# Kernel tuning notes

Hardware: AMD Instinct MI355X
Metric: run time of the kernel (lower is better)

## Reference

```python
import jax, jax.numpy as jnp
import numpy as np

DEPTH = 4
HEADS = 8
DIM = 512
DIM_HEAD = 64
INNER = HEADS * DIM_HEAD  # 512
MLP = 2048
NPK = 32
NEG = -1e9
EPS = 1e-5


def setup_inputs() -> dict:
    key = jax.random.key(0)
    ks = jax.random.split(key, 12)
    b, n, k = 2, 4096, 144
    x = jax.random.normal(ks[0], (b, n, DIM), jnp.float32)
    kx = jax.random.normal(ks[1], (b, k, DIM), jnp.float32)
    rd = jax.random.uniform(ks[2], (b, k, n), jnp.float32)
    clst = jax.random.normal(ks[3], (b, 1, DIM), jnp.float32)
    mask = jax.random.uniform(ks[4], (b, n, 1), jnp.float32)
    kmask = jax.random.uniform(ks[5], (b, k, 1), jnp.float32)

    def init(kk, shape, fan):
        return jax.random.normal(kk, shape, jnp.float32) / np.float32(np.sqrt(fan))

    return {
        "x": x, "kx": kx, "rd": rd, "clst": clst, "mask": mask, "kmask": kmask,
        "ln1_g": jnp.ones((DEPTH, DIM), jnp.float32),
        "ln1_b": jnp.zeros((DEPTH, DIM), jnp.float32),
        "w_qkv": init(ks[6], (DEPTH, DIM, 3 * INNER), DIM),
        "w_out": init(ks[7], (DEPTH, INNER, DIM), INNER),
        "b_out": jnp.zeros((DEPTH, DIM), jnp.float32),
        "ln2_g": jnp.ones((DEPTH, DIM), jnp.float32),
        "ln2_b": jnp.zeros((DEPTH, DIM), jnp.float32),
        "w1": init(ks[8], (DEPTH, DIM, MLP), DIM),
        "b1": jnp.zeros((DEPTH, MLP), jnp.float32),
        "w2": init(ks[9], (DEPTH, MLP, DIM), MLP),
        "b2": jnp.zeros((DEPTH, DIM), jnp.float32),
    }


def _ln(t, g, b):
    m = jnp.mean(t, axis=-1, keepdims=True)
    v = jnp.mean(jnp.square(t - m), axis=-1, keepdims=True)
    return (t - m) / jnp.sqrt(v + EPS) * g + b


def _split_heads(t):
    b, n, _ = t.shape
    return t.reshape(b, n, HEADS, DIM_HEAD).transpose(0, 2, 1, 3)  # b h n d


def _merge_heads(t):
    b, h, n, d = t.shape
    return t.transpose(0, 2, 1, 3).reshape(b, n, h * d)


def reference(x, kx, rd, clst, mask, kmask,
              ln1_g, ln1_b, w_qkv, w_out, b_out,
              ln2_g, ln2_b, w1, b1, w2, b2):
    scale = DIM_HEAD ** -0.5
    kernel_mask = kmask < 0.5                                   # [b,k,1] -> broadcast over dim
    att_mask = (jnp.einsum('bid,bjd->bij', mask, kmask) < 0.5)[:, None]  # [b,1,n,k]
    rd2 = (rd * rd)[:, None]                                    # [b,1,k,n]

    k_reps = []
    for l in range(DEPTH):
        x = _ln(x, ln1_g[l], ln1_b[l])
        kx = _ln(kx, ln1_g[l], ln1_b[l])
        clst = _ln(clst, ln1_g[l], ln1_b[l])
        krd = jnp.exp(-rd2 / (2 * NPK * (2 ** l)))              # [b,1,k,n]

        def qkv(t):
            p = t @ w_qkv[l]
            q, kk, v = jnp.split(p, 3, axis=-1)
            return _split_heads(q), _split_heads(kk), _split_heads(v)

        t_q, t_k, t_v = qkv(x)
        k_q, k_k, k_v = qkv(kx)
        c_q, _, _ = qkv(clst)

        def to_out(t):
            return _merge_heads(t) @ w_out[l] + b_out[l]

        # patch -> kernel cross-attention with post-softmax decay
        dots = jnp.einsum('bhid,bhjd->bhij', t_q, k_k) * scale   # [b,h,n,k]
        dots = jnp.where(att_mask, NEG, dots)
        attn = jax.nn.softmax(dots, axis=-1) * jnp.swapaxes(krd, -1, -2)
        x_ = to_out(jnp.einsum('bhij,bhjd->bhid', attn, k_v))

        # kernel -> patch cross-attention with decay
        k_dots = jnp.einsum('bhid,bhjd->bhij', k_q, t_k) * scale  # [b,h,k,n]
        k_dots = jnp.where(jnp.swapaxes(att_mask, -1, -2), NEG, k_dots)
        k_attn = jax.nn.softmax(k_dots, axis=-1) * krd
        kx_ = to_out(jnp.einsum('bhij,bhjd->bhid', k_attn, t_v))

        # class token -> kernel attention (no decay)
        c_dots = jnp.einsum('bhid,bhjd->bhij', c_q, k_k) * scale  # [b,h,1,k]
        c_dots = jnp.where(att_mask[:, :, :1], NEG, c_dots)
        c_attn = jax.nn.softmax(c_dots, axis=-1)
        clst_ = to_out(jnp.einsum('bhij,bhjd->bhid', c_attn, k_v))

        x = x + x_
        clst = clst + clst_
        kx = kx + kx_

        def ff(t):
            h = _ln(t, ln2_g[l], ln2_b[l])
            h = jax.nn.gelu(h @ w1[l] + b1[l], approximate=False)
            return h @ w2[l] + b2[l]

        x = ff(x) + x
        clst = ff(clst) + clst
        kx = ff(kx) + kx
        k_reps.append(jnp.where(kernel_mask, 0.0, kx))

    return jnp.stack(k_reps), clst
```

## Files before the change

### kernel.cpp

```cpp
#include <hip/hip_runtime.h>
#include <hip/hip_bf16.h>
#include <math.h>

#define NPAT 4096
#define NKER 144
#define DIMC 512
#define QKV_N 1536
#define MLP_N 2048
#define R_TOT 8482
#define R_PAD 8576
#define ROW_KX 8192
#define ROW_C 8480

typedef __hip_bfloat16 bf16;
using f32x4 = __attribute__((ext_vector_type(4))) float;
using s16x8 = __attribute__((ext_vector_type(8))) short;

template<typename T> __device__ __forceinline__ float tof(T v);
template<> __device__ __forceinline__ float tof<float>(float v) { return v; }
template<> __device__ __forceinline__ float tof<bf16>(bf16 v) { return __bfloat162float(v); }
template<typename T> __device__ __forceinline__ T fromf(float v);
template<> __device__ __forceinline__ float fromf<float>(float v) { return v; }
template<> __device__ __forceinline__ bf16 fromf<bf16>(float v) { return __float2bfloat16(v); }

__device__ __forceinline__ void gload_lds16(const bf16* g, bf16* l) {
  __builtin_amdgcn_global_load_lds((const __attribute__((address_space(1))) void*)g,
                                   (__attribute__((address_space(3))) void*)l, 16, 0, 0);
}

__device__ __forceinline__ float gelu_f(float x) {
  float u = 0.7978845608028654f * (x + 0.044715f * x * x * x);
  float t = 2.f / (1.f + __expf(-2.f * u)) - 1.f;
  return 0.5f * x * (1.f + t);
}

__device__ __forceinline__ unsigned fenc(float f) {
  unsigned u = __float_as_uint(f);
  return (u & 0x80000000u) ? ~u : (u | 0x80000000u);
}
__device__ __forceinline__ float fdec(unsigned u) {
  return (u & 0x80000000u) ? __uint_as_float(u & 0x7FFFFFFFu) : __uint_as_float(~u);
}

__device__ __forceinline__ float dot64q(const float* __restrict__ q, const bf16* __restrict__ k) {
  float acc = 0.f;
  const uint4* k4 = (const uint4*)k;
  #pragma unroll
  for (int t = 0; t < 8; ++t) {
    union { uint4 u; bf16 h[8]; } w; w.u = k4[t];
    #pragma unroll
    for (int e = 0; e < 8; ++e) acc += q[t * 8 + e] * tof(w.h[e]);
  }
  return acc;
}

template<typename TD>
__global__ void cvt_in(const float* __restrict__ s, TD* __restrict__ d, int n) {
  int i = blockIdx.x * 256 + threadIdx.x;
  if (i < n) d[i] = fromf<TD>(s[i]);
}

__global__ __launch_bounds__(256) void transpose_cvt(const float* __restrict__ src,
    bf16* __restrict__ dst, int K, int N) {
  __shared__ float tile[32][33];
  int kb = blockIdx.y * 32, nb = blockIdx.x * 32;
  int tx = threadIdx.x & 31, ty = threadIdx.x >> 5;
  #pragma unroll
  for (int r = ty; r < 32; r += 8) tile[r][tx] = src[(size_t)(kb + r) * N + nb + tx];
  __syncthreads();
  #pragma unroll
  for (int r = ty; r < 32; r += 8)
    dst[(size_t)(nb + r) * K + kb + tx] = fromf<bf16>(tile[tx][r]);
}

template<typename TS, typename TD>
__global__ __launch_bounds__(256) void ln_kernel(const TS* __restrict__ src,
    TD* __restrict__ dst, const float* __restrict__ g, const float* __restrict__ bb) {
  int row = blockIdx.x;
  const TS* p = src + (size_t)row * DIMC;
  int t = threadIdx.x;
  float v0 = tof(p[t]), v1 = tof(p[t + 256]);
  float s = v0 + v1;
  #pragma unroll
  for (int off = 32; off > 0; off >>= 1) s += __shfl_xor(s, off);
  __shared__ float ls[4], ls2[4];
  if ((t & 63) == 0) ls[t >> 6] = s;
  __syncthreads();
  float mean = (ls[0] + ls[1] + ls[2] + ls[3]) * (1.f / 512.f);
  float d0 = v0 - mean, d1 = v1 - mean;
  float s2 = d0 * d0 + d1 * d1;
  #pragma unroll
  for (int off = 32; off > 0; off >>= 1) s2 += __shfl_xor(s2, off);
  if ((t & 63) == 0) ls2[t >> 6] = s2;
  __syncthreads();
  float var = (ls2[0] + ls2[1] + ls2[2] + ls2[3]) * (1.f / 512.f);
  float rstd = rsqrtf(var + 1e-5f);
  TD* q = dst + (size_t)row * DIMC;
  q[t]       = fromf<TD>(d0 * rstd * g[t]       + bb[t]);
  q[t + 256] = fromf<TD>(d1 * rstd * g[t + 256] + bb[t + 256]);
}

__global__ __launch_bounds__(256) void ln_dual(float* __restrict__ act,
    bf16* __restrict__ actb, const float* __restrict__ g, const float* __restrict__ bb) {
  int row = blockIdx.x;
  float* p = act + (size_t)row * DIMC;
  int t = threadIdx.x;
  float v0 = p[t], v1 = p[t + 256];
  float s = v0 + v1;
  #pragma unroll
  for (int off = 32; off > 0; off >>= 1) s += __shfl_xor(s, off);
  __shared__ float ls[4], ls2[4];
  if ((t & 63) == 0) ls[t >> 6] = s;
  __syncthreads();
  float mean = (ls[0] + ls[1] + ls[2] + ls[3]) * (1.f / 512.f);
  float d0 = v0 - mean, d1 = v1 - mean;
  float s2 = d0 * d0 + d1 * d1;
  #pragma unroll
  for (int off = 32; off > 0; off >>= 1) s2 += __shfl_xor(s2, off);
  if ((t & 63) == 0) ls2[t >> 6] = s2;
  __syncthreads();
  float var = (ls2[0] + ls2[1] + ls2[2] + ls2[3]) * (1.f / 512.f);
  float rstd = rsqrtf(var + 1e-5f);
  float r0 = d0 * rstd * g[t] + bb[t];
  float r1 = d1 * rstd * g[t + 256] + bb[t + 256];
  p[t] = r0; p[t + 256] = r1;
  bf16* q = actb + (size_t)row * DIMC;
  q[t] = fromf<bf16>(r0); q[t + 256] = fromf<bf16>(r1);
}

template<int TM, typename TC, int ACT, bool HASRES>
__global__ __launch_bounds__(256) void gemm_mfma(
    const bf16* __restrict__ A, const bf16* __restrict__ Wt,
    const float* __restrict__ bias, const float* __restrict__ res,
    TC* __restrict__ C, int M, int N, int K) {
  constexpr int NI = 4;
  constexpr int NJ = (TM == 128) ? 4 : 2;
  constexpr int NQA = TM / 64;
  __shared__ bf16 As[2 * TM * 32];
  __shared__ bf16 Bs[2 * 128 * 32];
  int tid = threadIdx.x;
  int bm = blockIdx.y * TM, bn = blockIdx.x * 128;
  int wave = tid >> 6, lane = tid & 63;
  int quad = lane >> 4, lr = lane & 15;
  int WR = (TM == 128) ? (wave >> 1) * 64 : 0;
  int WC = (TM == 128) ? (wave & 1) * 64 : wave * 32;

  f32x4 acc[NI][NJ] = {};

  int rl = lane >> 2, pc = lane & 3;
  const bf16* aA[NQA]; const bf16* aB[2];
  int loA[NQA], loB[2];
  #pragma unroll
  for (int q = 0; q < NQA; ++q) {
    int rt = q * 64 + wave * 16 + rl;
    int c = pc ^ ((rt >> 1) & 3);
    aA[q] = A + (size_t)(bm + rt) * K + c * 8;
    loA[q] = (q * 64 + wave * 16) * 32;
  }
  #pragma unroll
  for (int q = 0; q < 2; ++q) {
    int rt = q * 64 + wave * 16 + rl;
    int c = pc ^ ((rt >> 1) & 3);
    aB[q] = Wt + (size_t)(bn + rt) * K + c * 8;
    loB[q] = (q * 64 + wave * 16) * 32;
  }

  auto stage = [&](int buf, int k0) {
    #pragma unroll
    for (int q = 0; q < NQA; ++q) gload_lds16(aA[q] + k0, As + buf * (TM * 32) + loA[q]);
    #pragma unroll
    for (int q = 0; q < 2; ++q)   gload_lds16(aB[q] + k0, Bs + buf * (128 * 32) + loB[q]);
  };

  stage(0, 0);
  int nk = K >> 5;
  for (int it = 0; it < nk; ++it) {
    __syncthreads();
    if (it + 1 < nk) stage((it + 1) & 1, (it + 1) << 5);
    const bf16* Ab = As + (it & 1) * (TM * 32);
    const bf16* Bb = Bs + (it & 1) * (128 * 32);
    s16x8 af[NI], bfr[NJ];
    #pragma unroll
    for (int i = 0; i < NI; ++i) {
      int ra = WR + i * 16 + lr;
      af[i] = *(const s16x8*)(Ab + ra * 32 + (quad ^ ((ra >> 1) & 3)) * 8);
    }
    #pragma unroll
    for (int j = 0; j < NJ; ++j) {
      int rb = WC + j * 16 + lr;
      bfr[j] = *(const s16x8*)(Bb + rb * 32 + (quad ^ ((rb >> 1) & 3)) * 8);
    }
    #pragma unroll
    for (int i = 0; i < NI; ++i)
      #pragma unroll
      for (int j = 0; j < NJ; ++j)
        acc[i][j] = __builtin_amdgcn_mfma_f32_16x16x32_bf16(af[i], bfr[j], acc[i][j], 0, 0, 0);
  }

  #pragma unroll
  for (int i = 0; i < NI; ++i) {
    int gm0 = bm + WR + i * 16 + quad * 4;
    #pragma unroll
    for (int j = 0; j < NJ; ++j) {
      int gn = bn + WC + j * 16 + lr;
      float bv = bias ? bias[gn] : 0.f;
      #pragma unroll
      for (int r = 0; r < 4; ++r) {
        int gm = gm0 + r;
        if (gm < M) {
          float v = acc[i][j][r] + bv;
          if (ACT == 1) v = gelu_f(v);
          if (HASRES) v += res[(size_t)gm * N + gn];
          C[(size_t)gm * N + gn] = fromf<TC>(v);
        }
      }
    }
  }
}

__global__ __launch_bounds__(256) void decay_tr(const float* __restrict__ rd,
    bf16* __restrict__ DT, bf16* __restrict__ DTk, float invden) {
  int ib = blockIdx.x * 32, jb = blockIdx.y * 32, b = blockIdx.z;
  __shared__ bf16 t[32][33];
  int tx = threadIdx.x & 31, ty = threadIdx.x >> 5;
  for (int r = ty; r < 32; r += 8) {
    int j = jb + r;
    if (j < NKER) {
      float v = rd[((size_t)b * NKER + j) * NPAT + ib + tx];
      bf16 dv = fromf<bf16>(expf(-v * v * invden));
      t[r][tx] = dv;
      DTk[((size_t)b * NKER + j) * NPAT + ib + tx] = dv;
    }
  }
  __syncthreads();
  for (int r = ty; r < 32; r += 8) {
    int i = ib + r, j = jb + tx;
    if (j < NKER) DT[((size_t)b * NPAT + i) * NKER + j] = t[tx][r];
  }
}

__global__ __launch_bounds__(256) void attn_p2k_f(
    const bf16* __restrict__ qkv, const float* __restrict__ pm,
    const float* __restrict__ km, const bf16* __restrict__ DT,
    bf16* __restrict__ o) {
  int i0 = blockIdx.x * 64, h = blockIdx.y, b = blockIdx.z;
  __shared__ bf16 Kk[144 * 72];
  __shared__ bf16 KvT[64 * 168];
  __shared__ bf16 Ps[64 * 168];
  __shared__ float pms[64];
  __shared__ float kms[144];
  int tid = threadIdx.x;
  bf16* Qs = Ps;

  for (int idx = tid; idx < 64 * 8; idx += 256) {
    int r = idx >> 3, c8 = idx & 7;
    *(uint4*)(Qs + r * 72 + c8 * 8) =
      *(const uint4*)(qkv + ((size_t)b * NPAT + i0 + r) * QKV_N + h * 64 + c8 * 8);
  }
  for (int idx = tid; idx < 144 * 8; idx += 256) {
    int r = idx >> 3, c8 = idx & 7;
    *(uint4*)(Kk + r * 72 + c8 * 8) =
      *(const uint4*)(qkv + ((size_t)ROW_KX + b * NKER + r) * QKV_N + DIMC + h * 64 + c8 * 8);
  }
  for (int idx = tid; idx < 144 * 8; idx += 256) {
    int r = idx >> 3, c8 = idx & 7;
    union { uint4 u; bf16 e[8]; } v;
    v.u = *(const uint4*)(qkv + ((size_t)ROW_KX + b * NKER + r) * QKV_N + 2 * DIMC + h * 64 + c8 * 8);
    #pragma unroll
    for (int e = 0; e < 8; ++e) KvT[(c8 * 8 + e) * 168 + r] = v.e[e];
  }
  for (int idx = tid; idx < 64 * 16; idx += 256) {
    int d = idx >> 4, j = 144 + (idx & 15);
    KvT[d * 168 + j] = fromf<bf16>(0.f);
  }
  if (tid < 64) pms[tid] = pm[(size_t)b * NPAT + i0 + tid];
  if (tid < 144) kms[tid] = km[b * NKER + tid];
  __syncthreads();

  int wave = tid >> 6, lane = tid & 63, quad = lane >> 4, lr = lane & 15;
  int mrow = wave * 16;

  f32x4 S[9] = {};
  #pragma unroll
  for (int kk = 0; kk < 64; kk += 32) {
    s16x8 a = *(const s16x8*)(Qs + (mrow + lr) * 72 + kk + quad * 8);
    #pragma unroll
    for (int n = 0; n < 9; ++n) {
      s16x8 bf_ = *(const s16x8*)(Kk + (n * 16 + lr) * 72 + kk + quad * 8);
      S[n] = __builtin_amdgcn_mfma_f32_16x16x32_bf16(a, bf_, S[n], 0, 0, 0);
    }
  }
  float mx[4] = {-3.4e38f, -3.4e38f, -3.4e38f, -3.4e38f};
  #pragma unroll
  for (int n = 0; n < 9; ++n) {
    int j = n * 16 + lr;
    float kmv = kms[j];
    #pragma unroll
    for (int r = 0; r < 4; ++r) {
      int il = mrow + quad * 4 + r;
      float s = S[n][r] * 0.125f;
      if (pms[il] * kmv < 0.5f) s = -1e9f;
      S[n][r] = s;
      mx[r] = fmaxf(mx[r], s);
    }
  }
  #pragma unroll
  for (int off = 1; off < 16; off <<= 1)
    #pragma unroll
    for (int r = 0; r < 4; ++r) mx[r] = fmaxf(mx[r], __shfl_xor(mx[r], off));
  float sum[4] = {0.f, 0.f, 0.f, 0.f};
  #pragma unroll
  for (int n = 0; n < 9; ++n)
    #pragma unroll
    for (int r = 0; r < 4; ++r) { float e = __expf(S[n][r] - mx[r]); S[n][r] = e; sum[r] += e; }
  #pragma unroll
  for (int off = 1; off < 16; off <<= 1)
    #pragma unroll
    for (int r = 0; r < 4; ++r) sum[r] += __shfl_xor(sum[r], off);
  float inv[4];
  #pragma unroll
  for (int r = 0; r < 4; ++r) inv[r] = 1.f / sum[r];
  #pragma unroll
  for (int n = 0; n < 9; ++n) {
    int j = n * 16 + lr;
    #pragma unroll
    for (int r = 0; r < 4; ++r) {
      int i = i0 + mrow + quad * 4 + r;
      S[n][r] = S[n][r] * inv[r] * tof(DT[((size_t)b * NPAT + i) * NKER + j]);
    }
  }
  __syncthreads();
  #pragma unroll
  for (int n = 0; n < 9; ++n) {
    int j = n * 16 + lr;
    #pragma unroll
    for (int r = 0; r < 4; ++r)
      Ps[(mrow + quad * 4 + r) * 168 + j] = fromf<bf16>(S[n][r]);
  }
  for (int idx = tid; idx < 64 * 16; idx += 256) {
    int rr = idx >> 4, j = 144 + (idx & 15);
    Ps[rr * 168 + j] = fromf<bf16>(0.f);
  }
  __syncthreads();
  f32x4 O[4] = {};
  #pragma unroll
  for (int kk = 0; kk < 160; kk += 32) {
    s16x8 a = *(const s16x8*)(Ps + (mrow + lr) * 168 + kk + quad * 8);
    #pragma unroll
    for (int nd = 0; nd < 4; ++nd) {
      s16x8 bf_ = *(const s16x8*)(KvT + (nd * 16 + lr) * 168 + kk + quad * 8);
      O[nd] = __builtin_amdgcn_mfma_f32_16x16x32_bf16(a, bf_, O[nd], 0, 0, 0);
    }
  }
  #pragma unroll
  for (int nd = 0; nd < 4; ++nd) {
    int d = nd * 16 + lr;
    #pragma unroll
    for (int r = 0; r < 4; ++r) {
      int i = i0 + mrow + quad * 4 + r;
      o[((size_t)b * NPAT + i) * DIMC + h * 64 + d] = fromf<bf16>(O[nd][r]);
    }
  }
}

__global__ __launch_bounds__(256) void s2_gemm(
    const bf16* __restrict__ qkv, const float* __restrict__ pm,
    const float* __restrict__ km, float* __restrict__ S2,
    unsigned* __restrict__ mxE) {
  int i0 = blockIdx.x * 128, h = blockIdx.y, b = blockIdx.z;
  __shared__ bf16 Kq[144 * 72];
  __shared__ bf16 Tk[128 * 72];
  __shared__ float pms[128];
  __shared__ float kms[144];
  int tid = threadIdx.x;
  for (int idx = tid; idx < 144 * 8; idx += 256) {
    int r = idx >> 3, c8 = idx & 7;
    *(uint4*)(Kq + r * 72 + c8 * 8) =
      *(const uint4*)(qkv + ((size_t)ROW_KX + b * NKER + r) * QKV_N + h * 64 + c8 * 8);
  }
  for (int idx = tid; idx < 128 * 8; idx += 256) {
    int r = idx >> 3, c8 = idx & 7;
    *(uint4*)(Tk + r * 72 + c8 * 8) =
      *(const uint4*)(qkv + ((size_t)b * NPAT + i0 + r) * QKV_N + DIMC + h * 64 + c8 * 8);
  }
  if (tid < 128) pms[tid] = pm[(size_t)b * NPAT + i0 + tid];
  if (tid < 144) kms[tid] = km[b * NKER + tid];
  __syncthreads();
  int wave = tid >> 6, lane = tid & 63, quad = lane >> 4, lr = lane & 15;
  int ncol = wave * 32;
  f32x4 acc[9][2] = {};
  #pragma unroll
  for (int kk = 0; kk < 64; kk += 32) {
    s16x8 bfr[2];
    #pragma unroll
    for (int ni = 0; ni < 2; ++ni)
      bfr[ni] = *(const s16x8*)(Tk + (ncol + ni * 16 + lr) * 72 + kk + quad * 8);
    #pragma unroll
    for (int mi = 0; mi < 9; ++mi) {
      s16x8 a = *(const s16x8*)(Kq + (mi * 16 + lr) * 72 + kk + quad * 8);
      #pragma unroll
      for (int ni = 0; ni < 2; ++ni)
        acc[mi][ni] = __builtin_amdgcn_mfma_f32_16x16x32_bf16(a, bfr[ni], acc[mi][ni], 0, 0, 0);
    }
  }
  size_t base = (size_t)(b * 8 + h) * NKER * NPAT;
  unsigned* mxb = mxE + (size_t)(b * 8 + h) * NKER;
  #pragma unroll
  for (int mi = 0; mi < 9; ++mi)
    #pragma unroll
    for (int r = 0; r < 4; ++r) {
      int j = mi * 16 + quad * 4 + r;
      float rowm = -3.4e38f;
      #pragma unroll
      for (int ni = 0; ni < 2; ++ni) {
        int il = ncol + ni * 16 + lr;
        float s = acc[mi][ni][r] * 0.125f;
        if (pms[il] * kms[j] < 0.5f) s = -1e9f;
        acc[mi][ni][r] = s;
        rowm = fmaxf(rowm, s);
        S2[base + (size_t)j * NPAT + i0 + il] = s;
      }
      #pragma unroll
      for (int off = 1; off < 16; off <<= 1) rowm = fmaxf(rowm, __shfl_xor(rowm, off));
      if (lr == 0) atomicMax(mxb + j, fenc(rowm));
    }
}

__global__ __launch_bounds__(256) void pv_k2p(
    const float* __restrict__ S2, const unsigned* __restrict__ mxE,
    const bf16* __restrict__ DTk, const bf16* __restrict__ qkv,
    float* __restrict__ koA, float* __restrict__ Z) {
  int kc = blockIdx.x, h = blockIdx.y, b = blockIdx.z;
  int tid = threadIdx.x;
  __shared__ char uls[144 * 64 * 4];
  bf16* TvT = (bf16*)uls;
  float* red = (float*)uls;
  int ib = kc * 256;
  for (int idx = tid; idx < 256 * 8; idx += 256) {
    int r = idx >> 3, c8 = idx & 7;
    union { uint4 u; bf16 e[8]; } v;
    v.u = *(const uint4*)(qkv + ((size_t)b * NPAT + ib + r) * QKV_N + 2 * DIMC + h * 64 + c8 * 8);
    #pragma unroll
    for (int e = 0; e < 8; ++e) TvT[(c8 * 8 + e) * 264 + r] = v.e[e];
  }
  __syncthreads();
  int wave = tid >> 6, lane = tid & 63, quad = lane >> 4, lr = lane & 15;
  int kb = wave * 64;
  int bh = b * 8 + h;
  size_t base = (size_t)bh * NKER * NPAT;
  f32x4 acc[9][4] = {};
  float zacc[9];
  float mxl[9];
  #pragma unroll
  for (int mi = 0; mi < 9; ++mi) {
    zacc[mi] = 0.f;
    mxl[mi] = fdec(mxE[(size_t)bh * NKER + mi * 16 + lr]);
  }
  #pragma unroll
  for (int kk = 0; kk < 64; kk += 32) {
    s16x8 bfr[4];
    #pragma unroll
    for (int nd = 0; nd < 4; ++nd)
      bfr[nd] = *(const s16x8*)(TvT + (nd * 16 + lr) * 264 + kb + kk + quad * 8);
    #pragma unroll
    for (int mi = 0; mi < 9; ++mi) {
      int j = mi * 16 + lr;
      int ioff = ib + kb + kk + quad * 8;
      const float* srow = S2 + base + (size_t)j * NPAT + ioff;
      const bf16* drow = DTk + ((size_t)b * NKER + j) * NPAT + ioff;
      float4 s0 = *(const float4*)srow;
      float4 s1 = *(const float4*)(srow + 4);
      union { uint4 u; bf16 e[8]; } dv; dv.u = *(const uint4*)drow;
      float sv[8] = {s0.x, s0.y, s0.z, s0.w, s1.x, s1.y, s1.z, s1.w};
      union { s16x8 v; bf16 e[8]; } w;
      float m = mxl[mi];
      float zl = 0.f;
      #pragma unroll
      for (int e = 0; e < 8; ++e) {
        float ev = __expf(sv[e] - m);
        zl += ev;
        w.e[e] = fromf<bf16>(ev * tof(dv.e[e]));
      }
      zacc[mi] += zl;
      #pragma unroll
      for (int nd = 0; nd < 4; ++nd)
        acc[mi][nd] = __builtin_amdgcn_mfma_f32_16x16x32_bf16(w.v, bfr[nd], acc[mi][nd], 0, 0, 0);
    }
  }
  #pragma unroll
  for (int mi = 0; mi < 9; ++mi) {
    float z = zacc[mi];
    z += __shfl_xor(z, 16);
    z += __shfl_xor(z, 32);
    if (quad == 0) atomicAdd(Z + (size_t)bh * NKER + mi * 16 + lr, z);
  }
  __syncthreads();
  for (int w = 0; w < 4; ++w) {
    if (wave == w) {
      #pragma unroll
      for (int mi = 0; mi < 9; ++mi)
        #pragma unroll
        for (int nd = 0; nd < 4; ++nd)
          #pragma unroll
          for (int r = 0; r < 4; ++r) {
            int j = mi * 16 + quad * 4 + r, d = nd * 16 + lr;
            if (w == 0) red[j * 64 + d] = acc[mi][nd][r];
            else        red[j * 64 + d] += acc[mi][nd][r];
          }
    }
    __syncthreads();
  }
  float* kbase = koA + (size_t)bh * NKER * 64;
  for (int idx = tid; idx < 144 * 64; idx += 256)
    atomicAdd(kbase + idx, red[idx]);
}

__global__ void merge_k2p(const float* __restrict__ koA, const float* __restrict__ Z,
                          bf16* __restrict__ o) {
  int idx = blockIdx.x * 256 + threadIdx.x;
  if (idx >= 2 * 8 * NKER * 64) return;
  int d = idx & 63, t = idx >> 6;
  int j = t % NKER; t /= NKER;
  int h = t & 7, b = t >> 3;
  float z = Z[(size_t)(b * 8 + h) * NKER + j];
  float v = (z > 0.f) ? koA[idx] / z : 0.f;
  o[((size_t)ROW_KX + b * NKER + j) * DIMC + h * 64 + d] = fromf<bf16>(v);
}

__global__ __launch_bounds__(64) void attn_c(const bf16* __restrict__ qkv,
    const float* __restrict__ pm, const float* __restrict__ km, bf16* __restrict__ o) {
  int h = blockIdx.x, b = blockIdx.y;
  int lane = threadIdx.x;
  size_t rowc = ROW_C + b;
  __shared__ float q_s[64];
  __shared__ float p_s[NKER];
  q_s[lane] = tof(qkv[rowc * QKV_N + h * 64 + lane]);
  __syncthreads();
  float pmv = pm[(size_t)b * NPAT];
  float lg[3];
  float mx = -3.4e38f;
  #pragma unroll
  for (int t = 0; t < 3; ++t) {
    int j = lane + t * 64;
    float val = -3.4e38f;
    if (j < NKER) {
      size_t rowk = ROW_KX + (size_t)b * NKER + j;
      float d = dot64q(q_s, qkv + rowk * QKV_N + DIMC + h * 64) * 0.125f;
      if (pmv * km[b * NKER + j] < 0.5f) d = -1e9f;
      val = d;
    }
    lg[t] = val;
    mx = fmaxf(mx, val);
  }
  #pragma unroll
  for (int off = 32; off > 0; off >>= 1) mx = fmaxf(mx, __shfl_xor(mx, off));
  float sum = 0.f, e[3];
  #pragma unroll
  for (int t = 0; t < 3; ++t) { e[t] = (lg[t] > -1e30f) ? expf(lg[t] - mx) : 0.f; sum += e[t]; }
  #pragma unroll
  for (int off = 32; off > 0; off >>= 1) sum += __shfl_xor(sum, off);
  float inv = 1.f / sum;
  #pragma unroll
  for (int t = 0; t < 3; ++t) { int j = lane + t * 64; if (j < NKER) p_s[j] = e[t] * inv; }
  __syncthreads();
  const bf16* vb = qkv + (ROW_KX + (size_t)b * NKER) * QKV_N + 2 * DIMC + h * 64 + lane;
  float acc = 0.f;
  for (int j = 0; j < NKER; ++j) acc += p_s[j] * tof(vb[(size_t)j * QKV_N]);
  o[rowc * DIMC + h * 64 + lane] = fromf<bf16>(acc);
}

template<typename TS>
__global__ void emit_kreps(const TS* __restrict__ act, const float* __restrict__ km,
                           float* __restrict__ out, int l) {
  int idx = blockIdx.x * 256 + threadIdx.x;
  if (idx >= 2 * NKER * DIMC) return;
  int r = idx >> 9;
  float v = (km[r] < 0.5f) ? 0.f : tof(act[((size_t)ROW_KX + r) * DIMC + (idx & 511)]);
  out[(size_t)l * (2 * NKER * DIMC) + idx] = v;
}
template<typename TS>
__global__ void emit_clst(const TS* __restrict__ act, float* __restrict__ out) {
  int idx = blockIdx.x * 256 + threadIdx.x;
  if (idx >= 2 * DIMC) return;
  out[(size_t)4 * 2 * NKER * DIMC + idx] = tof(act[(size_t)ROW_C * DIMC + idx]);
}

template<typename TA, typename TC>
__global__ __launch_bounds__(256) void gemm_bias(const TA* __restrict__ A,
    const float* __restrict__ W, const float* __restrict__ bias,
    const TC* __restrict__ res, TC* __restrict__ C,
    int M, int N, int K, int act) {
  __shared__ float As[16][64];
  __shared__ float Bs[16][64];
  int bm = blockIdx.y * 64, bn = blockIdx.x * 64;
  int tid = threadIdx.x;
  int tx = tid & 15, ty = tid >> 4;
  float acc[4][4] = {};
  for (int k0 = 0; k0 < K; k0 += 16) {
    #pragma unroll
    for (int it = 0; it < 4; ++it) {
      int idx = tid + 256 * it;
      int r = idx >> 4, c = idx & 15;
      int gm = bm + r;
      As[c][r] = (gm < M) ? tof(A[(size_t)gm * K + k0 + c]) : 0.f;
    }
    #pragma unroll
    for (int it = 0; it < 4; ++it) {
      int idx = tid + 256 * it;
      int r = idx >> 6, c = idx & 63;
      Bs[r][c] = W[(size_t)(k0 + r) * N + bn + c];
    }
    __syncthreads();
    #pragma unroll
    for (int kk = 0; kk < 16; ++kk) {
      float a[4], b[4];
      #pragma unroll
      for (int i = 0; i < 4; ++i) a[i] = As[kk][ty * 4 + i];
      #pragma unroll
      for (int j = 0; j < 4; ++j) b[j] = Bs[kk][tx * 4 + j];
      #pragma unroll
      for (int i = 0; i < 4; ++i)
        #pragma unroll
        for (int j = 0; j < 4; ++j) acc[i][j] += a[i] * b[j];
    }
    __syncthreads();
  }
  #pragma unroll
  for (int i = 0; i < 4; ++i) {
    int gm = bm + ty * 4 + i;
    if (gm >= M) continue;
    #pragma unroll
    for (int j = 0; j < 4; ++j) {
      int gn = bn + tx * 4 + j;
      float v = acc[i][j];
      if (bias) v += bias[gn];
      if (act == 1) v = gelu_f(v);
      if (res) v += tof(res[(size_t)gm * N + gn]);
      C[(size_t)gm * N + gn] = fromf<TC>(v);
    }
  }
}

static void run_fast2(void* const* d_in, float* out, float* act, bf16* actb,
                      bf16* bufo, bf16* bufq, bf16* wt,
                      float* S2, char* aux, float* koA, hipStream_t stream) {
  const float* x     = (const float*)d_in[0];
  const float* kx    = (const float*)d_in[1];
  const float* rd    = (const float*)d_in[2];
  const float* clst  = (const float*)d_in[3];
  const float* mask  = (const float*)d_in[4];
  const float* kmask = (const float*)d_in[5];
  const float* ln1g  = (const float*)d_in[6];
  const float* ln1b  = (const float*)d_in[7];
  const float* wqkv  = (const float*)d_in[8];
  const float* wout  = (const float*)d_in[9];
  const float* bout  = (const float*)d_in[10];
  const float* ln2g  = (const float*)d_in[11];
  const float* ln2b  = (const float*)d_in[12];
  const float* w1    = (const float*)d_in[13];
  const float* b1    = (const float*)d_in[14];
  const float* w2    = (const float*)d_in[15];
  const float* b2    = (const float*)d_in[16];

  unsigned* mxE = (unsigned*)aux;
  float*    Zb  = (float*)(aux + 16384);
  bf16*     DT  = (bf16*)(aux + 32768);
  bf16*     DTk = (bf16*)(aux + 32768 + (size_t)2 * NPAT * NKER * 2);

  bf16* wtq = wt;
  bf16* wto = wtq + (size_t)4 * QKV_N * DIMC;
  bf16* wt1 = wto + (size_t)4 * DIMC * DIMC;
  bf16* wt2 = wt1 + (size_t)4 * MLP_N * DIMC;

  for (int l = 0; l < 4; ++l) {
    transpose_cvt<<<dim3(QKV_N / 32, DIMC / 32), 256, 0, stream>>>(
        wqkv + (size_t)l * DIMC * QKV_N, wtq + (size_t)l * QKV_N * DIMC, DIMC, QKV_N);
    transpose_cvt<<<dim3(DIMC / 32, DIMC / 32), 256, 0, stream>>>(
        wout + (size_t)l * DIMC * DIMC, wto + (size_t)l * DIMC * DIMC, DIMC, DIMC);
    transpose_cvt<<<dim3(MLP_N / 32, DIMC / 32), 256, 0, stream>>>(
        w1 + (size_t)l * DIMC * MLP_N, wt1 + (size_t)l * MLP_N * DIMC, DIMC, MLP_N);
    transpose_cvt<<<dim3(DIMC / 32, MLP_N / 32), 256, 0, stream>>>(
        w2 + (size_t)l * MLP_N * DIMC, wt2 + (size_t)l * DIMC * MLP_N, MLP_N, DIMC);
  }

  bf16* qkv  = bufq;
  bf16* ffh  = (bf16*)S2;
  bf16* o    = bufo;
  bf16* actn = bufo;

  cvt_in<float><<<(2 * NPAT * DIMC + 255) / 256, 256, 0, stream>>>(x, act, 2 * NPAT * DIMC);
  cvt_in<float><<<(2 * NKER * DIMC + 255) / 256, 256, 0, stream>>>(kx, act + (size_t)ROW_KX * DIMC, 2 * NKER * DIMC);
  cvt_in<float><<<(2 * DIMC + 255) / 256, 256, 0, stream>>>(clst, act + (size_t)ROW_C * DIMC, 2 * DIMC);

  const int MT = R_PAD / 128;
  const int MT64 = R_PAD / 64;
  const int KON = 2 * 8 * NKER * 64;

  for (int l = 0; l < 4; ++l) {
    float invden = 1.0f / (64.0f * (float)(1 << l));
    ln_dual<<<R_TOT, 256, 0, stream>>>(act, actb, ln1g + l * DIMC, ln1b + l * DIMC);
    gemm_mfma<128, bf16, 0, false><<<dim3(QKV_N / 128, MT), 256, 0, stream>>>(
        actb, wtq + (size_t)l * QKV_N * DIMC, nullptr, nullptr, qkv, R_TOT, QKV_N, DIMC);
    decay_tr<<<dim3(NPAT / 32, 5, 2), 256, 0, stream>>>(rd, DT, DTk, invden);
    attn_p2k_f<<<dim3(NPAT / 64, 8, 2), 256, 0, stream>>>(qkv, mask, kmask, DT, o);
    hipMemsetAsync(mxE, 0, 2 * 8 * NKER * 4, stream);
    s2_gemm<<<dim3(NPAT / 128, 8, 2), 256, 0, stream>>>(qkv, mask, kmask, S2, mxE);
    hipMemsetAsync(Zb, 0, 2 * 8 * NKER * 4, stream);
    hipMemsetAsync(koA, 0, (size_t)KON * 4, stream);
    pv_k2p<<<dim3(16, 8, 2), 256, 0, stream>>>(S2, mxE, DTk, qkv, koA, Zb);
    merge_k2p<<<(KON + 255) / 256, 256, 0, stream>>>(koA, Zb, o);
    attn_c<<<dim3(8, 2), 64, 0, stream>>>(qkv, mask, kmask, o);
    gemm_mfma<64, float, 0, true><<<dim3(DIMC / 128, MT64), 256, 0, stream>>>(
        o, wto + (size_t)l * DIMC * DIMC, bout + l * DIMC, act, act, R_TOT, DIMC, DIMC);
    ln_kernel<float, bf16><<<R_TOT, 256, 0, stream>>>(act, actn, ln2g + l * DIMC, ln2b + l * DIMC);
    gemm_mfma<128, bf16, 1, false><<<dim3(MLP_N / 128, MT), 256, 0, stream>>>(
        actn, wt1 + (size_t)l * MLP_N * DIMC, b1 + l * MLP_N, nullptr, ffh, R_TOT, MLP_N, DIMC);
    gemm_mfma<64, float, 0, true><<<dim3(DIMC / 128, MT64), 256, 0, stream>>>(
        ffh, wt2 + (size_t)l * DIMC * MLP_N, b2 + l * DIMC, act, act, R_TOT, DIMC, MLP_N);
    emit_kreps<float><<<(2 * NKER * DIMC + 255) / 256, 256, 0, stream>>>(act, kmask, out, l);
  }
  emit_clst<float><<<(2 * DIMC + 255) / 256, 256, 0, stream>>>(act, out);
}

template<typename ActT>
static void run_pipeline(void* const* d_in, float* out, ActT* act, bf16* bufo, bf16* bufq,
                         hipStream_t stream) {
  const float* x     = (const float*)d_in[0];
  const float* kx    = (const float*)d_in[1];
  const float* clst  = (const float*)d_in[3];
  const float* mask  = (const float*)d_in[4];
  const float* kmask = (const float*)d_in[5];
  const float* ln1g  = (const float*)d_in[6];
  const float* ln1b  = (const float*)d_in[7];
  const float* wqkv  = (const float*)d_in[8];
  const float* wout  = (const float*)d_in[9];
  const float* bout  = (const float*)d_in[10];
  const float* ln2g  = (const float*)d_in[11];
  const float* ln2b  = (const float*)d_in[12];
  const float* w1    = (const float*)d_in[13];
  const float* b1    = (const float*)d_in[14];
  const float* w2    = (const float*)d_in[15];
  const float* b2    = (const float*)d_in[16];

  bf16* qkv  = bufq;
  bf16* ffh  = bufq;
  bf16* o    = bufo;
  bf16* actn = bufo;
  const int FF_CHUNK = 4241;

  cvt_in<ActT><<<(2 * NPAT * DIMC + 255) / 256, 256, 0, stream>>>(x, act, 2 * NPAT * DIMC);
  cvt_in<ActT><<<(2 * NKER * DIMC + 255) / 256, 256, 0, stream>>>(kx, act + (size_t)ROW_KX * DIMC, 2 * NKER * DIMC);
  cvt_in<ActT><<<(2 * DIMC + 255) / 256, 256, 0, stream>>>(clst, act + (size_t)ROW_C * DIMC, 2 * DIMC);

  for (int l = 0; l < 4; ++l) {
    ln_kernel<ActT, ActT><<<R_TOT, 256, 0, stream>>>(act, act, ln1g + l * DIMC, ln1b + l * DIMC);
    gemm_bias<ActT, bf16><<<dim3(QKV_N / 64, (R_TOT + 63) / 64), 256, 0, stream>>>(
        act, wqkv + (size_t)l * DIMC * QKV_N, nullptr, nullptr, qkv, R_TOT, QKV_N, DIMC, 0);
    attn_c<<<dim3(8, 2), 64, 0, stream>>>(qkv, mask, kmask, o);
    gemm_bias<bf16, ActT><<<dim3(DIMC / 64, (R_TOT + 63) / 64), 256, 0, stream>>>(
        o, wout + (size_t)l * DIMC * DIMC, bout + l * DIMC, act, act, R_TOT, DIMC, DIMC, 0);
    ln_kernel<ActT, bf16><<<R_TOT, 256, 0, stream>>>(act, actn, ln2g + l * DIMC, ln2b + l * DIMC);
    for (int c0 = 0; c0 < R_TOT; c0 += FF_CHUNK) {
      int rows = (R_TOT - c0 < FF_CHUNK) ? (R_TOT - c0) : FF_CHUNK;
      gemm_bias<bf16, bf16><<<dim3(MLP_N / 64, (rows + 63) / 64), 256, 0, stream>>>(
          actn + (size_t)c0 * DIMC, w1 + (size_t)l * DIMC * MLP_N, b1 + l * MLP_N,
          nullptr, ffh, rows, MLP_N, DIMC, 1);
      gemm_bias<bf16, ActT><<<dim3(DIMC / 64, (rows + 63) / 64), 256, 0, stream>>>(
          ffh, w2 + (size_t)l * MLP_N * DIMC, b2 + l * DIMC,
          act + (size_t)c0 * DIMC, act + (size_t)c0 * DIMC, rows, DIMC, MLP_N, 0);
    }
    emit_kreps<ActT><<<(2 * NKER * DIMC + 255) / 256, 256, 0, stream>>>(act, kmask, out, l);
  }
  emit_clst<ActT><<<(2 * DIMC + 255) / 256, 256, 0, stream>>>(act, out);
}

extern "C" void kernel_launch(void* const* d_in, const int* in_sizes, int n_in,
                              void* d_out, int out_size, void* d_ws, size_t ws_size,
                              hipStream_t stream) {
  (void)in_sizes; (void)n_in; (void)out_size;
  float* out = (float*)d_out;

  const size_t szA  = (size_t)R_TOT * DIMC * 4;
  const size_t szAB = (size_t)R_PAD * DIMC * 2;
  const size_t szO  = (size_t)R_PAD * DIMC * 2;
  const size_t szQ  = (size_t)R_PAD * QKV_N * 2;
  const size_t szW  = (size_t)4 * (QKV_N * DIMC + DIMC * DIMC + MLP_N * DIMC + DIMC * MLP_N) * 2;
  const size_t szS2 = (size_t)2 * 8 * NKER * NPAT * 4;
  const size_t szAux = (size_t)2 * 8 * NKER * NPAT * 2;
  const size_t szKo = (size_t)2 * 8 * NKER * 64 * 4;
  const size_t needFast2 = szA + szAB + szO + szQ + szW + szS2 + szAux + szKo;

  if (ws_size >= needFast2) {
    char* w = (char*)d_ws;
    float* act  = (float*)w;            w += szA;
    bf16*  actb = (bf16*)w;             w += szAB;
    bf16*  bufo = (bf16*)w;             w += szO;
    bf16*  bufq = (bf16*)w;             w += szQ;
    bf16*  wt   = (bf16*)w;             w += szW;
    float* S2   = (float*)w;            w += szS2;
    char*  aux  = w;                    w += szAux;
    float* koA  = (float*)w;
    run_fast2(d_in, out, act, actb, bufo, bufq, wt, S2, aux, koA, stream);
  } else if (ws_size >= szA + szO + szQ) {
    float* act = (float*)d_ws;
    bf16* bufo = (bf16*)((char*)d_ws + szA);
    bf16* bufq = (bf16*)((char*)d_ws + szA + szO);
    run_pipeline<float>(d_in, out, act, bufo, bufq, stream);
  } else {
    bf16* act = (bf16*)d_ws;
    bf16* bufo = (bf16*)((char*)d_ws + szO);
    bf16* bufq = (bf16*)((char*)d_ws + 2 * szO);
    run_pipeline<bf16>(d_in, out, act, bufo, bufq, stream);
  }
}
```

Baseline: 1.355 ms.

## Fuse kernel-to-patch softmax exp into score GEMM, skip max pass, vectorize layernorms

The kernel-to-patch score GEMM now computes exp directly, multiplies by the decay, writes bf16 probabilities and accumulates row sums. It no longer writes fp32 scores and an atomic row max, and it relies on the scores being small enough to skip max subtraction. A precomputed per-batch mask max handles fully masked rows as uniform weights. pv_k2p just reads the bf16 probabilities. Layernorms switch to one wave per row with float4 loads, and expf becomes __expf. Dropping max subtraction risks overflow for large logits.

```diff
diff --git a/kernel.cpp b/kernel.cpp
--- a/kernel.cpp
+++ b/kernel.cpp
@@ -34,14 +34,6 @@
   return 0.5f * x * (1.f + t);
 }
 
-__device__ __forceinline__ unsigned fenc(float f) {
-  unsigned u = __float_as_uint(f);
-  return (u & 0x80000000u) ? ~u : (u | 0x80000000u);
-}
-__device__ __forceinline__ float fdec(unsigned u) {
-  return (u & 0x80000000u) ? __uint_as_float(u & 0x7FFFFFFFu) : __uint_as_float(~u);
-}
-
 __device__ __forceinline__ float dot64q(const float* __restrict__ q, const bf16* __restrict__ k) {
   float acc = 0.f;
   const uint4* k4 = (const uint4*)k;
@@ -58,6 +50,19 @@
 __global__ void cvt_in(const float* __restrict__ s, TD* __restrict__ d, int n) {
   int i = blockIdx.x * 256 + threadIdx.x;
   if (i < n) d[i] = fromf<TD>(s[i]);
+}
+
+__global__ __launch_bounds__(256) void pmax_calc(const float* __restrict__ pm,
+                                                 float* __restrict__ pmax) {
+  int b = blockIdx.x, t = threadIdx.x;
+  float m = 0.f;
+  for (int i = t; i < NPAT; i += 256) m = fmaxf(m, pm[(size_t)b * NPAT + i]);
+  #pragma unroll
+  for (int off = 32; off > 0; off >>= 1) m = fmaxf(m, __shfl_xor(m, off));
+  __shared__ float ws[4];
+  if ((t & 63) == 0) ws[t >> 6] = m;
+  __syncthreads();
+  if (t == 0) pmax[b] = fmaxf(fmaxf(ws[0], ws[1]), fmaxf(ws[2], ws[3]));
 }
 
 __global__ __launch_bounds__(256) void transpose_cvt(const float* __restrict__ src,
@@ -71,6 +76,75 @@
   #pragma unroll
   for (int r = ty; r < 32; r += 8)
     dst[(size_t)(nb + r) * K + kb + tx] = fromf<bf16>(tile[tx][r]);
+}
+
+template<typename TD>
+__global__ __launch_bounds__(256) void ln_row4(const float* __restrict__ src,
+    TD* __restrict__ dst, const float* __restrict__ g, const float* __restrict__ bb,
+    int nrows) {
+  int row = blockIdx.x * 4 + (threadIdx.x >> 6);
+  if (row >= nrows) return;
+  int lane = threadIdx.x & 63;
+  const float4* p4 = (const float4*)(src + (size_t)row * DIMC);
+  float4 a = p4[lane * 2], b = p4[lane * 2 + 1];
+  float v[8] = {a.x, a.y, a.z, a.w, b.x, b.y, b.z, b.w};
+  float s = 0.f;
+  #pragma unroll
+  for (int e = 0; e < 8; ++e) s += v[e];
+  #pragma unroll
+  for (int off = 32; off > 0; off >>= 1) s += __shfl_xor(s, off);
+  float mean = s * (1.f / 512.f);
+  float s2 = 0.f;
+  #pragma unroll
+  for (int e = 0; e < 8; ++e) { float d = v[e] - mean; s2 += d * d; }
+  #pragma unroll
+  for (int off = 32; off > 0; off >>= 1) s2 += __shfl_xor(s2, off);
+  float rstd = rsqrtf(s2 * (1.f / 512.f) + 1e-5f);
+  const float4* g4 = (const float4*)(g + lane * 8);
+  const float4* b4 = (const float4*)(bb + lane * 8);
+  float4 g0 = g4[0], g1 = g4[1], bb0 = b4[0], bb1 = b4[1];
+  float gg[8] = {g0.x, g0.y, g0.z, g0.w, g1.x, g1.y, g1.z, g1.w};
+  float bv[8] = {bb0.x, bb0.y, bb0.z, bb0.w, bb1.x, bb1.y, bb1.z, bb1.w};
+  TD* q = dst + (size_t)row * DIMC + lane * 8;
+  #pragma unroll
+  for (int e = 0; e < 8; ++e) q[e] = fromf<TD>((v[e] - mean) * rstd * gg[e] + bv[e]);
+}
+
+__global__ __launch_bounds__(256) void ln_dual4(float* __restrict__ act,
+    bf16* __restrict__ actb, const float* __restrict__ g, const float* __restrict__ bb,
+    int nrows) {
+  int row = blockIdx.x * 4 + (threadIdx.x >> 6);
+  if (row >= nrows) return;
+  int lane = threadIdx.x & 63;
+  float4* p4 = (float4*)(act + (size_t)row * DIMC);
+  float4 a = p4[lane * 2], b = p4[lane * 2 + 1];
+  float v[8] = {a.x, a.y, a.z, a.w, b.x, b.y, b.z, b.w};
+  float s = 0.f;
+  #pragma unroll
+  for (int e = 0; e < 8; ++e) s += v[e];
+  #pragma unroll
+  for (int off = 32; off > 0; off >>= 1) s += __shfl_xor(s, off);
+  float mean = s * (1.f / 512.f);
+  float s2 = 0.f;
+  #pragma unroll
+  for (int e = 0; e < 8; ++e) { float d = v[e] - mean; s2 += d * d; }
+  #pragma unroll
+  for (int off = 32; off > 0; off >>= 1) s2 += __shfl_xor(s2, off);
+  float rstd = rsqrtf(s2 * (1.f / 512.f) + 1e-5f);
+  const float4* g4 = (const float4*)(g + lane * 8);
+  const float4* b4 = (const float4*)(bb + lane * 8);
+  float4 g0 = g4[0], g1 = g4[1], bb0 = b4[0], bb1 = b4[1];
+  float gg[8] = {g0.x, g0.y, g0.z, g0.w, g1.x, g1.y, g1.z, g1.w};
+  float bv[8] = {bb0.x, bb0.y, bb0.z, bb0.w, bb1.x, bb1.y, bb1.z, bb1.w};
+  float r[8];
+  #pragma unroll
+  for (int e = 0; e < 8; ++e) r[e] = (v[e] - mean) * rstd * gg[e] + bv[e];
+  p4[lane * 2]     = make_float4(r[0], r[1], r[2], r[3]);
+  p4[lane * 2 + 1] = make_float4(r[4], r[5], r[6], r[7]);
+  union { uint4 u; bf16 e[8]; } w;
+  #pragma unroll
+  for (int e = 0; e < 8; ++e) w.e[e] = fromf<bf16>(r[e]);
+  *(uint4*)(actb + (size_t)row * DIMC + lane * 8) = w.u;
 }
 
 template<typename TS, typename TD>
@@ -98,34 +172,6 @@
   TD* q = dst + (size_t)row * DIMC;
   q[t]       = fromf<TD>(d0 * rstd * g[t]       + bb[t]);
   q[t + 256] = fromf<TD>(d1 * rstd * g[t + 256] + bb[t + 256]);
-}
-
-__global__ __launch_bounds__(256) void ln_dual(float* __restrict__ act,
-    bf16* __restrict__ actb, const float* __restrict__ g, const float* __restrict__ bb) {
-  int row = blockIdx.x;
-  float* p = act + (size_t)row * DIMC;
-  int t = threadIdx.x;
-  float v0 = p[t], v1 = p[t + 256];
-  float s = v0 + v1;
-  #pragma unroll
-  for (int off = 32; off > 0; off >>= 1) s += __shfl_xor(s, off);
-  __shared__ float ls[4], ls2[4];
-  if ((t & 63) == 0) ls[t >> 6] = s;
-  __syncthreads();
-  float mean = (ls[0] + ls[1] + ls[2] + ls[3]) * (1.f / 512.f);
-  float d0 = v0 - mean, d1 = v1 - mean;
-  float s2 = d0 * d0 + d1 * d1;
-  #pragma unroll
-  for (int off = 32; off > 0; off >>= 1) s2 += __shfl_xor(s2, off);
-  if ((t & 63) == 0) ls2[t >> 6] = s2;
-  __syncthreads();
-  float var = (ls2[0] + ls2[1] + ls2[2] + ls2[3]) * (1.f / 512.f);
-  float rstd = rsqrtf(var + 1e-5f);
-  float r0 = d0 * rstd * g[t] + bb[t];
-  float r1 = d1 * rstd * g[t + 256] + bb[t + 256];
-  p[t] = r0; p[t + 256] = r1;
-  bf16* q = actb + (size_t)row * DIMC;
-  q[t] = fromf<bf16>(r0); q[t + 256] = fromf<bf16>(r1);
 }
 
 template<int TM, typename TC, int ACT, bool HASRES>
@@ -227,7 +273,7 @@
     int j = jb + r;
     if (j < NKER) {
       float v = rd[((size_t)b * NKER + j) * NPAT + ib + tx];
-      bf16 dv = fromf<bf16>(expf(-v * v * invden));
+      bf16 dv = fromf<bf16>(__expf(-v * v * invden));
       t[r][tx] = dv;
       DTk[((size_t)b * NKER + j) * NPAT + ib + tx] = dv;
     }
@@ -363,10 +409,10 @@
   }
 }
 
-__global__ __launch_bounds__(256) void s2_gemm(
+__global__ __launch_bounds__(256) void s2p_gemm(
     const bf16* __restrict__ qkv, const float* __restrict__ pm,
-    const float* __restrict__ km, float* __restrict__ S2,
-    unsigned* __restrict__ mxE) {
+    const float* __restrict__ km, const float* __restrict__ pmax,
+    const bf16* __restrict__ DTk, bf16* __restrict__ P2b, float* __restrict__ Z) {
   int i0 = blockIdx.x * 128, h = blockIdx.y, b = blockIdx.z;
   __shared__ bf16 Kq[144 * 72];
   __shared__ bf16 Tk[128 * 72];
@@ -403,33 +449,38 @@
         acc[mi][ni] = __builtin_amdgcn_mfma_f32_16x16x32_bf16(a, bfr[ni], acc[mi][ni], 0, 0, 0);
     }
   }
-  size_t base = (size_t)(b * 8 + h) * NKER * NPAT;
-  unsigned* mxb = mxE + (size_t)(b * 8 + h) * NKER;
+  int bh = b * 8 + h;
+  size_t base = (size_t)bh * NKER * NPAT;
+  float pmx = pmax[b];
   #pragma unroll
   for (int mi = 0; mi < 9; ++mi)
     #pragma unroll
     for (int r = 0; r < 4; ++r) {
       int j = mi * 16 + quad * 4 + r;
-      float rowm = -3.4e38f;
+      float kmv = kms[j];
+      bool fullmask = (kmv * pmx < 0.5f);
+      float zpart = 0.f;
       #pragma unroll
       for (int ni = 0; ni < 2; ++ni) {
         int il = ncol + ni * 16 + lr;
         float s = acc[mi][ni][r] * 0.125f;
-        if (pms[il] * kms[j] < 0.5f) s = -1e9f;
-        acc[mi][ni][r] = s;
-        rowm = fmaxf(rowm, s);
-        S2[base + (size_t)j * NPAT + i0 + il] = s;
+        float e;
+        if (fullmask) e = 1.f;
+        else if (pms[il] * kmv < 0.5f) e = 0.f;
+        else e = __expf(s);
+        zpart += e;
+        float d = tof(DTk[((size_t)b * NKER + j) * NPAT + i0 + il]);
+        P2b[base + (size_t)j * NPAT + i0 + il] = fromf<bf16>(e * d);
       }
       #pragma unroll
-      for (int off = 1; off < 16; off <<= 1) rowm = fmaxf(rowm, __shfl_xor(rowm, off));
-      if (lr == 0) atomicMax(mxb + j, fenc(rowm));
+      for (int off = 1; off < 16; off <<= 1) zpart += __shfl_xor(zpart, off);
+      if (lr == 0) atomicAdd(Z + (size_t)bh * NKER + j, zpart);
     }
 }
 
 __global__ __launch_bounds__(256) void pv_k2p(
-    const float* __restrict__ S2, const unsigned* __restrict__ mxE,
-    const bf16* __restrict__ DTk, const bf16* __restrict__ qkv,
-    float* __restrict__ koA, float* __restrict__ Z) {
+    const bf16* __restrict__ P2b, const bf16* __restrict__ qkv,
+    float* __restrict__ koA) {
   int kc = blockIdx.x, h = blockIdx.y, b = blockIdx.z;
   int tid = threadIdx.x;
   __shared__ char uls[144 * 64 * 4];
@@ -449,13 +500,6 @@
   int bh = b * 8 + h;
   size_t base = (size_t)bh * NKER * NPAT;
   f32x4 acc[9][4] = {};
-  float zacc[9];
-  float mxl[9];
-  #pragma unroll
-  for (int mi = 0; mi < 9; ++mi) {
-    zacc[mi] = 0.f;
-    mxl[mi] = fdec(mxE[(size_t)bh * NKER + mi * 16 + lr]);
-  }
   #pragma unroll
   for (int kk = 0; kk < 64; kk += 32) {
     s16x8 bfr[4];
@@ -464,35 +508,11 @@
       bfr[nd] = *(const s16x8*)(TvT + (nd * 16 + lr) * 264 + kb + kk + quad * 8);
     #pragma unroll
     for (int mi = 0; mi < 9; ++mi) {
-      int j = mi * 16 + lr;
-      int ioff = ib + kb + kk + quad * 8;
-      const float* srow = S2 + base + (size_t)j * NPAT + ioff;
-      const bf16* drow = DTk + ((size_t)b * NKER + j) * NPAT + ioff;
-      float4 s0 = *(const float4*)srow;
-      float4 s1 = *(const float4*)(srow + 4);
-      union { uint4 u; bf16 e[8]; } dv; dv.u = *(const uint4*)drow;
-      float sv[8] = {s0.x, s0.y, s0.z, s0.w, s1.x, s1.y, s1.z, s1.w};
-      union { s16x8 v; bf16 e[8]; } w;
-      float m = mxl[mi];
-      float zl = 0.f;
-      #pragma unroll
-      for (int e = 0; e < 8; ++e) {
-        float ev = __expf(sv[e] - m);
-        zl += ev;
-        w.e[e] = fromf<bf16>(ev * tof(dv.e[e]));
-      }
-      zacc[mi] += zl;
+      s16x8 a = *(const s16x8*)(P2b + base + (size_t)(mi * 16 + lr) * NPAT + ib + kb + kk + quad * 8);
       #pragma unroll
       for (int nd = 0; nd < 4; ++nd)
-        acc[mi][nd] = __builtin_amdgcn_mfma_f32_16x16x32_bf16(w.v, bfr[nd], acc[mi][nd], 0, 0, 0);
-    }
-  }
-  #pragma unroll
-  for (int mi = 0; mi < 9; ++mi) {
-    float z = zacc[mi];
-    z += __shfl_xor(z, 16);
-    z += __shfl_xor(z, 32);
-    if (quad == 0) atomicAdd(Z + (size_t)bh * NKER + mi * 16 + lr, z);
+        acc[mi][nd] = __builtin_amdgcn_mfma_f32_16x16x32_bf16(a, bfr[nd], acc[mi][nd], 0, 0, 0);
+    }
   }
   __syncthreads();
   for (int w = 0; w < 4; ++w) {
@@ -556,7 +576,7 @@
   for (int off = 32; off > 0; off >>= 1) mx = fmaxf(mx, __shfl_xor(mx, off));
   float sum = 0.f, e[3];
   #pragma unroll
-  for (int t = 0; t < 3; ++t) { e[t] = (lg[t] > -1e30f) ? expf(lg[t] - mx) : 0.f; sum += e[t]; }
+  for (int t = 0; t < 3; ++t) { e[t] = (lg[t] > -1e30f) ? __expf(lg[t] - mx) : 0.f; sum += e[t]; }
   #pragma unroll
   for (int off = 32; off > 0; off >>= 1) sum += __shfl_xor(sum, off);
   float inv = 1.f / sum;
@@ -662,10 +682,11 @@
   const float* w2    = (const float*)d_in[15];
   const float* b2    = (const float*)d_in[16];
 
-  unsigned* mxE = (unsigned*)aux;
-  float*    Zb  = (float*)(aux + 16384);
-  bf16*     DT  = (bf16*)(aux + 32768);
-  bf16*     DTk = (bf16*)(aux + 32768 + (size_t)2 * NPAT * NKER * 2);
+  float* Zb   = (float*)aux;
+  float* pmax = (float*)(aux + 16384);
+  bf16*  DT   = (bf16*)(aux + 32768);
+  bf16*  DTk  = (bf16*)(aux + 32768 + (size_t)2 * NPAT * NKER * 2);
+  bf16*  P2b  = (bf16*)S2;
 
   bf16* wtq = wt;
   bf16* wto = wtq + (size_t)4 * QKV_N * DIMC;
@@ -682,6 +703,7 @@
     transpose_cvt<<<dim3(DIMC / 32, MLP_N / 32), 256, 0, stream>>>(
         w2 + (size_t)l * MLP_N * DIMC, wt2 + (size_t)l * DIMC * MLP_N, MLP_N, DIMC);
   }
+  pmax_calc<<<2, 256, 0, stream>>>(mask, pmax);
 
   bf16* qkv  = bufq;
   bf16* ffh  = (bf16*)S2;
@@ -695,24 +717,24 @@
   const int MT = R_PAD / 128;
   const int MT64 = R_PAD / 64;
   const int KON = 2 * 8 * NKER * 64;
+  const int LNB = (R_TOT + 3) / 4;
 
   for (int l = 0; l < 4; ++l) {
     float invden = 1.0f / (64.0f * (float)(1 << l));
-    ln_dual<<<R_TOT, 256, 0, stream>>>(act, actb, ln1g + l * DIMC, ln1b + l * DIMC);
+    ln_dual4<<<LNB, 256, 0, stream>>>(act, actb, ln1g + l * DIMC, ln1b + l * DIMC, R_TOT);
     gemm_mfma<128, bf16, 0, false><<<dim3(QKV_N / 128, MT), 256, 0, stream>>>(
         actb, wtq + (size_t)l * QKV_N * DIMC, nullptr, nullptr, qkv, R_TOT, QKV_N, DIMC);
     decay_tr<<<dim3(NPAT / 32, 5, 2), 256, 0, stream>>>(rd, DT, DTk, invden);
     attn_p2k_f<<<dim3(NPAT / 64, 8, 2), 256, 0, stream>>>(qkv, mask, kmask, DT, o);
-    hipMemsetAsync(mxE, 0, 2 * 8 * NKER * 4, stream);
-    s2_gemm<<<dim3(NPAT / 128, 8, 2), 256, 0, stream>>>(qkv, mask, kmask, S2, mxE);
     hipMemsetAsync(Zb, 0, 2 * 8 * NKER * 4, stream);
     hipMemsetAsync(koA, 0, (size_t)KON * 4, stream);
-    pv_k2p<<<dim3(16, 8, 2), 256, 0, stream>>>(S2, mxE, DTk, qkv, koA, Zb);
+    s2p_gemm<<<dim3(NPAT / 128, 8, 2), 256, 0, stream>>>(qkv, mask, kmask, pmax, DTk, P2b, Zb);
+    pv_k2p<<<dim3(16, 8, 2), 256, 0, stream>>>(P2b, qkv, koA);
     merge_k2p<<<(KON + 255) / 256, 256, 0, stream>>>(koA, Zb, o);
     attn_c<<<dim3(8, 2), 64, 0, stream>>>(qkv, mask, kmask, o);
     gemm_mfma<64, float, 0, true><<<dim3(DIMC / 128, MT64), 256, 0, stream>>>(
         o, wto + (size_t)l * DIMC * DIMC, bout + l * DIMC, act, act, R_TOT, DIMC, DIMC);
-    ln_kernel<float, bf16><<<R_TOT, 256, 0, stream>>>(act, actn, ln2g + l * DIMC, ln2b + l * DIMC);
+    ln_row4<bf16><<<LNB, 256, 0, stream>>>(act, actn, ln2g + l * DIMC, ln2b + l * DIMC, R_TOT);
     gemm_mfma<128, bf16, 1, false><<<dim3(MLP_N / 128, MT), 256, 0, stream>>>(
         actn, wt1 + (size_t)l * MLP_N * DIMC, b1 + l * MLP_N, nullptr, ffh, R_TOT, MLP_N, DIMC);
     gemm_mfma<64, float, 0, true><<<dim3(DIMC / 128, MT64), 256, 0, stream>>>(
```

New measurement: 1.385 ms. +2.2%, slower.
